# Kernel optimization log

Measured on AMD Instinct MI355X. Metric: run time of the kernel, lower is better.

Reference implementation:

```python
import jax, jax.numpy as jnp
import numpy as np


def _diff_argmax(hm_flat):
    # Mirrors DifferentiableArgmax.forward: 1-based flat argmax as float32.
    return jnp.argmax(hm_flat, axis=-1).astype(jnp.float32) + 1.0


def setup_inputs() -> dict:
    key = jax.random.key(0)
    k1, k2, k3 = jax.random.split(key, 3)
    B, C, H, W = 256, 68, 64, 64
    pred_hm = jax.random.normal(k1, (B, C, H, W), dtype=jnp.float32)
    # face centers somewhere inside a 1024x1024 image
    center = jax.random.uniform(k2, (B, 2), minval=300.0, maxval=700.0, dtype=jnp.float32)
    # typical face_alignment scale (bbox extent / reference_scale)
    scale = jax.random.uniform(k3, (B,), minval=1.5, maxval=3.0, dtype=jnp.float32)
    return {"pred_hm": pred_hm, "center": center, "scale": scale}


def reference(pred_hm, center, scale):
    B, C, H, W = pred_hm.shape
    idx = _diff_argmax(pred_hm.reshape(B, C, H * W))  # [B,C], 1-based
    px = (idx - 1.0) % W + 1.0                        # 1-based column
    py = jnp.floor((idx - 1.0) / H) + 1.0             # 1-based row

    # --- subpixel refine: sign of neighbor differences (non-differentiable in original) ---
    iX = px.astype(jnp.int32) - 1                     # 0-based
    iY = py.astype(jnp.int32) - 1
    iXc = jnp.clip(iX, 1, W - 2)
    iYc = jnp.clip(iY, 1, H - 2)
    b = jnp.arange(B)[:, None]
    c = jnp.arange(C)[None, :]
    dx = pred_hm[b, c, iYc, iXc + 1] - pred_hm[b, c, iYc, iXc - 1]
    dy = pred_hm[b, c, iYc + 1, iXc] - pred_hm[b, c, iYc - 1, iXc]
    interior = (iX > 0) & (iX < W - 1) & (iY > 0) & (iY < H - 1)
    px = px + jnp.where(interior, jnp.sign(dx) * 0.25, 0.0) - 0.5
    py = py + jnp.where(interior, jnp.sign(dy) * 0.25, 0.0) - 0.5

    # --- inverse affine transform (analytic inverse of transform()) ---
    # t = [[res/h,0,res*(-cx/h+.5)],[0,res/h,res*(-cy/h+.5)],[0,0,1]], h=200*scale
    # inv:  x' = x*h/res + cx - 0.5h ;  y' = y*h/res + cy - 0.5h   (res = H)
    h = 200.0 * scale[:, None]                        # [B,1]
    ox = px * (h / H) + center[:, 0:1] - 0.5 * h
    oy = py * (h / H) + center[:, 1:2] - 0.5 * h
    return jnp.stack([ox, oy], axis=-1)               # [B, 68, 2]
```

## Files before the change

kernel.cpp:

```cpp
#include <hip/hip_runtime.h>

#define BB 256
#define CC 68
#define HH 64
#define WW 64

__global__ __launch_bounds__(256) void face_landmark_kernel(
    const float* __restrict__ pred_hm,
    const float* __restrict__ center,
    const float* __restrict__ scale,
    float* __restrict__ out)
{
    const int bc = blockIdx.x;
    const int b  = bc / CC;
    const int tid = threadIdx.x;

    const float* hm = pred_hm + (size_t)bc * (HH * WW);
    const float4* hm4 = (const float4*)hm;

    float best_v = -__builtin_inff();
    int   best_i = 0;
#pragma unroll
    for (int k = 0; k < 4; ++k) {
        const int fi = tid + 256 * k;
        const float4 v = hm4[fi];
        const int base = fi * 4;
        if (v.x > best_v) { best_v = v.x; best_i = base;     }
        if (v.y > best_v) { best_v = v.y; best_i = base + 1; }
        if (v.z > best_v) { best_v = v.z; best_i = base + 2; }
        if (v.w > best_v) { best_v = v.w; best_i = base + 3; }
    }

#pragma unroll
    for (int off = 32; off > 0; off >>= 1) {
        const float ov = __shfl_down(best_v, off, 64);
        const int   oi = __shfl_down(best_i, off, 64);
        if (ov > best_v || (ov == best_v && oi < best_i)) { best_v = ov; best_i = oi; }
    }

    __shared__ float sv[4];
    __shared__ int   si[4];
    const int wave = tid >> 6;
    const int lane = tid & 63;
    if (lane == 0) { sv[wave] = best_v; si[wave] = best_i; }
    __syncthreads();

    if (tid == 0) {
#pragma unroll
        for (int w = 1; w < 4; ++w) {
            if (sv[w] > best_v || (sv[w] == best_v && si[w] < best_i)) {
                best_v = sv[w]; best_i = si[w];
            }
        }

        const int idx = best_i;
        const int iX = idx & (WW - 1);
        const int iY = idx >> 6;
        float px = (float)(iX + 1);
        float py = (float)(iY + 1);

        const bool interior = (iX > 0) && (iX < WW - 1) && (iY > 0) && (iY < HH - 1);
        if (interior) {
            const int iXc = iX < 1 ? 1 : (iX > WW - 2 ? WW - 2 : iX);
            const int iYc = iY < 1 ? 1 : (iY > HH - 2 ? HH - 2 : iY);
            const float dx = hm[iYc * WW + iXc + 1] - hm[iYc * WW + iXc - 1];
            const float dy = hm[(iYc + 1) * WW + iXc] - hm[(iYc - 1) * WW + iXc];
            px += (dx > 0.0f) ? 0.25f : ((dx < 0.0f) ? -0.25f : 0.0f);
            py += (dy > 0.0f) ? 0.25f : ((dy < 0.0f) ? -0.25f : 0.0f);
        }
        px -= 0.5f;
        py -= 0.5f;

        const float h  = 200.0f * scale[b];
        const float hr = h * (1.0f / (float)HH);
        const float ox = px * hr + center[b * 2 + 0] - 0.5f * h;
        const float oy = py * hr + center[b * 2 + 1] - 0.5f * h;

        ((float2*)out)[bc] = make_float2(ox, oy);
    }
}

extern "C" void kernel_launch(void* const* d_in, const int* in_sizes, int n_in,
                              void* d_out, int out_size, void* d_ws, size_t ws_size,
                              hipStream_t stream) {
    const float* pred_hm = (const float*)d_in[0];
    const float* center  = (const float*)d_in[1];
    const float* scale   = (const float*)d_in[2];
    float* out = (float*)d_out;

    face_landmark_kernel<<<dim3(BB * CC), dim3(256), 0, stream>>>(
        pred_hm, center, scale, out);
}
```

Baseline: 369.5 us.

## Assign one heatmap per wavefront with persistent grid-stride blocks

Each wavefront now owns a whole 64x64 heatmap and loops over channels in a grid-stride loop over a fixed grid of 544 blocks, instead of one 256-thread block per channel. Each lane issues 16 float4 loads up front before reducing. This removes the cross-wave shared-memory reduction and __syncthreads, and cuts per-block launch and scheduling overhead. The cost is higher register pressure and reliance on the fixed grid and per-wave memory parallelism to keep HBM bandwidth saturated.

```diff
diff --git a/kernel.cpp b/kernel.cpp
--- a/kernel.cpp
+++ b/kernel.cpp
@@ -4,6 +4,8 @@
 #define CC 68
 #define HH 64
 #define WW 64
+#define NCH (BB * CC)
+#define NBLK 544
 
 __global__ __launch_bounds__(256) void face_landmark_kernel(
     const float* __restrict__ pred_hm,
@@ -11,72 +13,61 @@
     const float* __restrict__ scale,
     float* __restrict__ out)
 {
-    const int bc = blockIdx.x;
-    const int b  = bc / CC;
-    const int tid = threadIdx.x;
+    const int lane = threadIdx.x & 63;
+    const int wave = blockIdx.x * 4 + (threadIdx.x >> 6);
+    const int nwaves = NBLK * 4;
 
-    const float* hm = pred_hm + (size_t)bc * (HH * WW);
-    const float4* hm4 = (const float4*)hm;
+    for (int ch = wave; ch < NCH; ch += nwaves) {
+        const float* hm = pred_hm + (size_t)ch * (HH * WW);
+        const float4* hm4 = (const float4*)hm;
 
-    float best_v = -__builtin_inff();
-    int   best_i = 0;
+        float4 v[16];
 #pragma unroll
-    for (int k = 0; k < 4; ++k) {
-        const int fi = tid + 256 * k;
-        const float4 v = hm4[fi];
-        const int base = fi * 4;
-        if (v.x > best_v) { best_v = v.x; best_i = base;     }
-        if (v.y > best_v) { best_v = v.y; best_i = base + 1; }
-        if (v.z > best_v) { best_v = v.z; best_i = base + 2; }
-        if (v.w > best_v) { best_v = v.w; best_i = base + 3; }
-    }
+        for (int k = 0; k < 16; ++k) v[k] = hm4[lane + 64 * k];
+
+        float best_v = -__builtin_inff();
+        int   best_i = 0;
+#pragma unroll
+        for (int k = 0; k < 16; ++k) {
+            const int base = (lane + 64 * k) * 4;
+            if (v[k].x > best_v) { best_v = v[k].x; best_i = base;     }
+            if (v[k].y > best_v) { best_v = v[k].y; best_i = base + 1; }
+            if (v[k].z > best_v) { best_v = v[k].z; best_i = base + 2; }
+            if (v[k].w > best_v) { best_v = v[k].w; best_i = base + 3; }
+        }
 
 #pragma unroll
-    for (int off = 32; off > 0; off >>= 1) {
-        const float ov = __shfl_down(best_v, off, 64);
-        const int   oi = __shfl_down(best_i, off, 64);
-        if (ov > best_v || (ov == best_v && oi < best_i)) { best_v = ov; best_i = oi; }
-    }
-
-    __shared__ float sv[4];
-    __shared__ int   si[4];
-    const int wave = tid >> 6;
-    const int lane = tid & 63;
-    if (lane == 0) { sv[wave] = best_v; si[wave] = best_i; }
-    __syncthreads();
-
-    if (tid == 0) {
-#pragma unroll
-        for (int w = 1; w < 4; ++w) {
-            if (sv[w] > best_v || (sv[w] == best_v && si[w] < best_i)) {
-                best_v = sv[w]; best_i = si[w];
-            }
+        for (int off = 32; off > 0; off >>= 1) {
+            const float ov = __shfl_down(best_v, off, 64);
+            const int   oi = __shfl_down(best_i, off, 64);
+            if (ov > best_v || (ov == best_v && oi < best_i)) { best_v = ov; best_i = oi; }
         }
 
-        const int idx = best_i;
-        const int iX = idx & (WW - 1);
-        const int iY = idx >> 6;
-        float px = (float)(iX + 1);
-        float py = (float)(iY + 1);
+        if (lane == 0) {
+            const int idx = best_i;
+            const int iX = idx & (WW - 1);
+            const int iY = idx >> 6;
+            float px = (float)(iX + 1);
+            float py = (float)(iY + 1);
 
-        const bool interior = (iX > 0) && (iX < WW - 1) && (iY > 0) && (iY < HH - 1);
-        if (interior) {
-            const int iXc = iX < 1 ? 1 : (iX > WW - 2 ? WW - 2 : iX);
-            const int iYc = iY < 1 ? 1 : (iY > HH - 2 ? HH - 2 : iY);
-            const float dx = hm[iYc * WW + iXc + 1] - hm[iYc * WW + iXc - 1];
-            const float dy = hm[(iYc + 1) * WW + iXc] - hm[(iYc - 1) * WW + iXc];
-            px += (dx > 0.0f) ? 0.25f : ((dx < 0.0f) ? -0.25f : 0.0f);
-            py += (dy > 0.0f) ? 0.25f : ((dy < 0.0f) ? -0.25f : 0.0f);
+            const bool interior = (iX > 0) && (iX < WW - 1) && (iY > 0) && (iY < HH - 1);
+            if (interior) {
+                const float dx = hm[iY * WW + iX + 1] - hm[iY * WW + iX - 1];
+                const float dy = hm[(iY + 1) * WW + iX] - hm[(iY - 1) * WW + iX];
+                px += (dx > 0.0f) ? 0.25f : ((dx < 0.0f) ? -0.25f : 0.0f);
+                py += (dy > 0.0f) ? 0.25f : ((dy < 0.0f) ? -0.25f : 0.0f);
+            }
+            px -= 0.5f;
+            py -= 0.5f;
+
+            const int b = ch / CC;
+            const float h  = 200.0f * scale[b];
+            const float hr = h * (1.0f / (float)HH);
+            const float ox = px * hr + center[b * 2 + 0] - 0.5f * h;
+            const float oy = py * hr + center[b * 2 + 1] - 0.5f * h;
+
+            ((float2*)out)[ch] = make_float2(ox, oy);
         }
-        px -= 0.5f;
-        py -= 0.5f;
-
-        const float h  = 200.0f * scale[b];
-        const float hr = h * (1.0f / (float)HH);
-        const float ox = px * hr + center[b * 2 + 0] - 0.5f * h;
-        const float oy = py * hr + center[b * 2 + 1] - 0.5f * h;
-
-        ((float2*)out)[bc] = make_float2(ox, oy);
     }
 }
 
@@ -88,6 +79,6 @@
     const float* scale   = (const float*)d_in[2];
     float* out = (float*)d_out;
 
-    face_landmark_kernel<<<dim3(BB * CC), dim3(256), 0, stream>>>(
+    face_landmark_kernel<<<dim3(NBLK), dim3(256), 0, stream>>>(
         pred_hm, center, scale, out);
 }
```

Measured after the change: 376.0 us. No clear change (+1.8%).
